# Optimization experiments

Measured on AMD Instinct MI355X. Metric: run time of the kernel, lower is better.

Reference implementation:

```python
import jax, jax.numpy as jnp
import numpy as np

B, S, D = 4, 2048, 1024
N_HEAD = 16
D_HEAD = D // N_HEAD
WINDOW = 1024
D_FF = 4 * D
EPS = 1e-5
NEG = -1e10


def _layernorm(x, g, b):
    mu = jnp.mean(x, axis=-1, keepdims=True)
    var = jnp.mean(jnp.square(x - mu), axis=-1, keepdims=True)
    return (x - mu) * jax.lax.rsqrt(var + EPS) * g + b


def setup_inputs() -> dict:
    key = jax.random.key(0)
    ks = jax.random.split(key, 12)
    s = 1.0 / np.sqrt(D)
    x = jax.random.normal(ks[0], (B, S, D), dtype=jnp.float32)
    key_pad_mask = jax.random.bernoulli(ks[1], 0.1, (B, S))
    return {
        "x": x,
        "key_pad_mask": key_pad_mask,
        "ln1_g": jnp.ones((D,), jnp.float32),
        "ln1_b": jnp.zeros((D,), jnp.float32),
        "wq": jax.random.normal(ks[2], (D, D), jnp.float32) * s,
        "bq": jnp.zeros((D,), jnp.float32),
        "wkv": jax.random.normal(ks[3], (D, 2 * D), jnp.float32) * s,
        "bkv": jnp.zeros((2 * D,), jnp.float32),
        "ln2_g": jnp.ones((D,), jnp.float32),
        "ln2_b": jnp.zeros((D,), jnp.float32),
        "w1": jax.random.normal(ks[4], (D, D_FF), jnp.float32) * s,
        "b1": jnp.zeros((D_FF,), jnp.float32),
        "w2": jax.random.normal(ks[5], (D_FF, D), jnp.float32) * (1.0 / np.sqrt(D_FF)),
        "b2": jnp.zeros((D,), jnp.float32),
    }


def reference(x, key_pad_mask, ln1_g, ln1_b, wq, bq, wkv, bkv, ln2_g, ln2_b, w1, b1, w2, b2):
    ln1x = _layernorm(x, ln1_g, ln1_b)
    # queries over full sequence: [B, S, nh, dh]
    q = (ln1x @ wq + bq).reshape(B, S, N_HEAD, D_HEAD)
    # keys/values from the last WINDOW tokens: [B, W, 2*nh, dh]
    kv = (ln1x[:, -WINDOW:, :] @ wkv + bkv).reshape(B, WINDOW, 2 * N_HEAD, D_HEAD)
    k, v = kv[..., :N_HEAD, :], kv[..., N_HEAD:, :]
    # NOTE: original scales by sqrt(embed_dim), not sqrt(head_dim)
    scores = jnp.einsum('bqhd,bkhd->bhqk', q, k) / np.sqrt(D)
    causal = jnp.triu(jnp.ones((S, WINDOW), dtype=bool), k=1)  # faithful to original
    pad = key_pad_mask[:, None, None, -WINDOW:]
    scores = jnp.where(pad | causal[None, None], jnp.float32(NEG), scores)
    attn = jax.nn.softmax(scores, axis=-1)
    out = jnp.einsum('bhqk,bkhd->bqhd', attn, v).reshape(B, S, D)
    h = _layernorm(out, ln2_g, ln2_b)
    h = jax.nn.silu(h @ w1 + b1) @ w2 + b2
    return h + x
```

## Files before the change

### kernel.cpp

```cpp
#include <hip/hip_runtime.h>
#include <hip/hip_bf16.h>

#define BB 4
#define SS 2048
#define DD 1024
#define HH 16
#define DHH 64
#define WW 1024
#define DFF 4096
#define MM (BB*SS)
#define NEGV (-1e10f)

using f32x4 = __attribute__((ext_vector_type(4))) float;
using s16x8 = __attribute__((ext_vector_type(8))) short;
using s16x4 = __attribute__((ext_vector_type(4))) short;

typedef const __attribute__((address_space(1))) void* gas_t;
typedef __attribute__((address_space(3))) void* las_t;

__device__ inline short f2b(float f) {
  __hip_bfloat16 h = __float2bfloat16(f);
  return __builtin_bit_cast(short, h);
}
__device__ inline float b2f(short u) {
  __hip_bfloat16 h = __builtin_bit_cast(__hip_bfloat16, u);
  return __bfloat162float(h);
}

__device__ inline void gload_lds16(const short* g, short* lds) {
  __builtin_amdgcn_global_load_lds((gas_t)g, (las_t)lds, 16, 0, 0);
}

__device__ inline f32x4 mfma16(s16x8 a, s16x8 b, f32x4 c) {
  return __builtin_amdgcn_mfma_f32_16x16x32_bf16(a, b, c, 0, 0, 0);
}

template<int IN_BF16>
__global__ __launch_bounds__(256) void ln_kernel(const void* __restrict__ inp,
                                                 const float* __restrict__ g,
                                                 const float* __restrict__ bta,
                                                 short* __restrict__ outp) {
  int row = blockIdx.x;
  int t = threadIdx.x;
  float v[4];
  if constexpr (IN_BF16) {
    s16x4 r4 = *((const s16x4*)((const short*)inp + (size_t)row*DD) + t);
    v[0]=b2f(r4[0]); v[1]=b2f(r4[1]); v[2]=b2f(r4[2]); v[3]=b2f(r4[3]);
  } else {
    f32x4 r4 = *((const f32x4*)((const float*)inp + (size_t)row*DD) + t);
    v[0]=r4[0]; v[1]=r4[1]; v[2]=r4[2]; v[3]=r4[3];
  }
  float s = v[0]+v[1]+v[2]+v[3];
  float sq = v[0]*v[0]+v[1]*v[1]+v[2]*v[2]+v[3]*v[3];
  for (int m=1;m<64;m<<=1){ s += __shfl_xor(s,m); sq += __shfl_xor(sq,m); }
  __shared__ float red[8];
  int wv = t>>6;
  if ((t&63)==0){ red[wv]=s; red[4+wv]=sq; }
  __syncthreads();
  s  = red[0]+red[1]+red[2]+red[3];
  sq = red[4]+red[5]+red[6]+red[7];
  float mean = s*(1.f/DD);
  float rstd = rsqrtf(sq*(1.f/DD) - mean*mean + 1e-5f);
  int col = t*4;
  s16x4 o;
  #pragma unroll
  for (int j=0;j<4;++j) o[j] = f2b((v[j]-mean)*rstd*g[col+j]+bta[col+j]);
  *((s16x4*)(outp + (size_t)row*DD) + t) = o;
}

__global__ __launch_bounds__(256) void transpose_cast(const float* __restrict__ in,
                                                      short* __restrict__ out,
                                                      int K, int N) {
  __shared__ float tile[32][33];
  int n0 = blockIdx.x*32, k0 = blockIdx.y*32;
  int tx = threadIdx.x & 31, ty = threadIdx.x >> 5;
  #pragma unroll
  for (int j=0;j<4;++j) tile[ty+8*j][tx] = in[(size_t)(k0+ty+8*j)*N + n0+tx];
  __syncthreads();
  #pragma unroll
  for (int j=0;j<4;++j) out[(size_t)(n0+ty+8*j)*K + k0+tx] = f2b(tile[tx][ty+8*j]);
}

template<int EPI>
__global__ __launch_bounds__(256) void gemm_bt(const short* __restrict__ A,
                                               const short* __restrict__ Bt,
                                               const float* __restrict__ bias,
                                               void* __restrict__ out1,
                                               void* __restrict__ out2,
                                               const float* __restrict__ resid,
                                               int N, int K) {
  __shared__ short As[128*32], Bs[128*32];
  int tid = threadIdx.x, l = tid&63;
  int wv = tid>>6, wm = wv>>1, wn = wv&1;
  int bx = blockIdx.x, by = blockIdx.y;
  const short* Ablk;
  if constexpr (EPI==1) {
    int b_ = (by*128)>>10;
    int w0 = (by*128)&1023;
    Ablk = A + ((size_t)b_*SS + (SS-WW) + w0)*DD;
  } else {
    Ablk = A + (size_t)by*128*K;
  }
  const short* Bblk = Bt + (size_t)bx*128*K;
  f32x4 acc[4][4];
  #pragma unroll
  for (int i=0;i<4;++i)
    #pragma unroll
    for(int j=0;j<4;++j)
      #pragma unroll
      for(int r=0;r<4;++r) acc[i][j][r]=0.f;
  int rA = l & 15;
  int cslot = (((l>>4) ^ ((l>>1)&3))*8);
  for (int kt=0; kt<K; kt+=32) {
    __syncthreads();
    #pragma unroll
    for (int p=0;p<2;++p) {
      int s = p*256 + tid;
      int srow = s>>2;
      int scs = (((s&3) ^ ((s>>3)&3))*8);
      gload_lds16(Ablk + (size_t)srow*K + kt + scs, &As[(p*256 + (tid & ~63))*8]);
      gload_lds16(Bblk + (size_t)srow*K + kt + scs, &Bs[(p*256 + (tid & ~63))*8]);
    }
    __syncthreads();
    s16x8 af[4], bfr[4];
    #pragma unroll
    for (int mf=0;mf<4;++mf) af[mf]  = *(const s16x8*)&As[(wm*64+mf*16+rA)*32 + cslot];
    #pragma unroll
    for (int nf=0;nf<4;++nf) bfr[nf] = *(const s16x8*)&Bs[(wn*64+nf*16+rA)*32 + cslot];
    #pragma unroll
    for (int mf=0;mf<4;++mf)
      #pragma unroll
      for (int nf=0;nf<4;++nf)
        acc[mf][nf] = mfma16(af[mf], bfr[nf], acc[mf][nf]);
  }
  #pragma unroll
  for (int mf=0;mf<4;++mf) {
    #pragma unroll
    for (int nf=0;nf<4;++nf) {
      #pragma unroll
      for (int r=0;r<4;++r) {
        int row = by*128 + wm*64 + mf*16 + ((l>>4)<<2) + r;
        int col = bx*128 + wn*64 + nf*16 + (l&15);
        float v = acc[mf][nf][r] + bias[col];
        if constexpr (EPI==0) {
          ((short*)out1)[(size_t)row*N + col] = f2b(v);
        } else if constexpr (EPI==1) {
          int b_ = row>>10, w_ = row&1023;
          if (col < DD) {
            int h = col>>6, dh = col&63;
            ((short*)out1)[(((size_t)(b_*HH+h))*WW + w_)*DHH + dh] = f2b(v);
          } else {
            int cc = col - DD;
            int h = cc>>6, dh = cc&63;
            ((short*)out2)[(((size_t)(b_*HH+h))*DHH + dh)*WW + w_] = f2b(v);
          }
        } else if constexpr (EPI==2) {
          float sv = v / (1.f + __expf(-v));
          ((short*)out1)[(size_t)row*N + col] = f2b(sv);
        } else {
          ((float*)out1)[(size_t)row*N + col] = v + resid[(size_t)row*N + col];
        }
      }
    }
  }
}

__global__ __launch_bounds__(256) void attn_kernel(const short* __restrict__ q,
    const short* __restrict__ kpan, const short* __restrict__ vtpan,
    const int* __restrict__ pad, short* __restrict__ outp) {
  __shared__ short Ks[64*64], Vts[64*64];
  __shared__ short P[4][16*72];
  int tid = threadIdx.x, l = tid&63, wv = tid>>6;
  int qt = blockIdx.x, h = blockIdx.y, bb = blockIdx.z;
  int s0 = qt*64;
  int srow0 = s0 + wv*16;
  const short* qbase = q + ((size_t)bb*SS + srow0 + (l&15))*DD + h*DHH + ((l>>4)*8);
  s16x8 aq0 = *(const s16x8*)qbase;
  s16x8 aq1 = *(const s16x8*)(qbase + 32);
  const short* kbase = kpan + (size_t)(bb*HH+h)*WW*DHH;
  const short* vbase = vtpan + (size_t)(bb*HH+h)*DHH*WW;
  const int* padb = pad + bb*SS + (SS-WW);
  f32x4 oacc[4];
  #pragma unroll
  for (int i=0;i<4;++i)
    #pragma unroll
    for (int r=0;r<4;++r) oacc[i][r]=0.f;
  float mrun[4], lrun[4];
  #pragma unroll
  for (int r=0;r<4;++r){ mrun[r]=-INFINITY; lrun[r]=0.f; }
  int nch = (qt+1 < 16) ? qt+1 : 16;

  auto body = [&](int c) {
    __syncthreads();
    #pragma unroll
    for (int p=0;p<2;++p) {
      int s = p*256 + tid;
      int row = s>>3;
      int scs = (((s&7) ^ (row&7))*8);
      gload_lds16(kbase + (size_t)(c*64+row)*DHH + scs, &Ks[(p*256 + (tid&~63))*8]);
      gload_lds16(vbase + (size_t)row*WW + c*64 + scs,  &Vts[(p*256 + (tid&~63))*8]);
    }
    __syncthreads();
    f32x4 sc[4];
    #pragma unroll
    for (int nf=0;nf<4;++nf)
      #pragma unroll
      for (int r=0;r<4;++r) sc[nf][r]=0.f;
    #pragma unroll
    for (int nf=0;nf<4;++nf) {
      int row = nf*16 + (l&15);
      s16x8 bk0 = *(const s16x8*)&Ks[row*64 + ((((l>>4)    ) ^ (l&7))*8)];
      s16x8 bk1 = *(const s16x8*)&Ks[row*64 + (((4 + (l>>4)) ^ (l&7))*8)];
      sc[nf] = mfma16(aq0, bk0, sc[nf]);
      sc[nf] = mfma16(aq1, bk1, sc[nf]);
    }
    float vals[4][4];
    float pm[4] = {-INFINITY,-INFINITY,-INFINITY,-INFINITY};
    #pragma unroll
    for (int nf=0;nf<4;++nf) {
      int j = c*64 + nf*16 + (l&15);
      int pd = padb[j];
      #pragma unroll
      for (int r=0;r<4;++r) {
        int sq_ = srow0 + ((l>>4)<<2) + r;
        float xv = (pd || (j > sq_)) ? NEGV : sc[nf][r]*0.03125f;
        vals[nf][r] = xv;
        pm[r] = fmaxf(pm[r], xv);
      }
    }
    #pragma unroll
    for (int m=1;m<16;m<<=1)
      #pragma unroll
      for (int r=0;r<4;++r) pm[r] = fmaxf(pm[r], __shfl_xor(pm[r], m));
    float scale[4], ls[4];
    #pragma unroll
    for (int r=0;r<4;++r) {
      float mn = fmaxf(mrun[r], pm[r]);
      scale[r] = __expf(mrun[r]-mn);
      mrun[r] = mn;
      ls[r] = 0.f;
    }
    #pragma unroll
    for (int nf=0;nf<4;++nf)
      #pragma unroll
      for (int r=0;r<4;++r) {
        float p_ = __expf(vals[nf][r]-mrun[r]);
        vals[nf][r]=p_; ls[r]+=p_;
      }
    #pragma unroll
    for (int m=1;m<16;m<<=1)
      #pragma unroll
      for (int r=0;r<4;++r) ls[r] += __shfl_xor(ls[r], m);
    #pragma unroll
    for (int r=0;r<4;++r) lrun[r] = lrun[r]*scale[r] + ls[r];
    #pragma unroll
    for (int nf=0;nf<4;++nf)
      #pragma unroll
      for (int r=0;r<4;++r) oacc[nf][r] *= scale[r];
    short* Pw = &P[wv][0];
    #pragma unroll
    for (int nf=0;nf<4;++nf)
      #pragma unroll
      for (int r=0;r<4;++r)
        Pw[(((l>>4)<<2)+r)*72 + nf*16 + (l&15)] = f2b(vals[nf][r]);
    #pragma unroll
    for (int ks=0;ks<2;++ks) {
      s16x8 ap = *(const s16x8*)&Pw[(l&15)*72 + ks*32 + ((l>>4)*8)];
      #pragma unroll
      for (int nf=0;nf<4;++nf) {
        int row = nf*16 + (l&15);
        s16x8 bv = *(const s16x8*)&Vts[row*64 + (((ks*4 + (l>>4)) ^ (l&7))*8)];
        oacc[nf] = mfma16(ap, bv, oacc[nf]);
      }
    }
  };

  for (int c=0;c<nch;++c) body(c);
  int dead = 0;
  #pragma unroll
  for (int r=0;r<4;++r) dead |= (mrun[r] < -5e9f) ? 1 : 0;
  if (__syncthreads_or(dead)) {
    for (int c=nch;c<16;++c) body(c);
  }
  #pragma unroll
  for (int nf=0;nf<4;++nf)
    #pragma unroll
    for (int r=0;r<4;++r) {
      int srow = srow0 + ((l>>4)<<2) + r;
      float o = oacc[nf][r] / lrun[r];
      outp[((size_t)bb*SS + srow)*DD + h*DHH + nf*16 + (l&15)] = f2b(o);
    }
}

extern "C" void kernel_launch(void* const* d_in, const int* in_sizes, int n_in,
                              void* d_out, int out_size, void* d_ws, size_t ws_size,
                              hipStream_t stream) {
  const float* x    = (const float*)d_in[0];
  const int*   pad  = (const int*)d_in[1];
  const float* ln1g = (const float*)d_in[2];
  const float* ln1b = (const float*)d_in[3];
  const float* wq   = (const float*)d_in[4];
  const float* bq   = (const float*)d_in[5];
  const float* wkv  = (const float*)d_in[6];
  const float* bkv  = (const float*)d_in[7];
  const float* ln2g = (const float*)d_in[8];
  const float* ln2b = (const float*)d_in[9];
  const float* w1   = (const float*)d_in[10];
  const float* b1   = (const float*)d_in[11];
  const float* w2   = (const float*)d_in[12];
  const float* b2   = (const float*)d_in[13];

  char* ws = (char*)d_ws;
  const size_t MB = 1024*1024;
  short* ln1x = (short*)(ws + 0);
  short* qb   = (short*)(ws + 16*MB);
  short* kpan = (short*)(ws + 32*MB);
  short* vtp  = (short*)(ws + 40*MB);
  short* h1   = (short*)(ws + 0);
  short* outb = (short*)(ws + 64*MB);
  short* hb   = (short*)(ws + 80*MB);
  short* wqT  = (short*)(ws + 96*MB);
  short* wkvT = (short*)(ws + 98*MB);
  short* w1T  = (short*)(ws + 102*MB);
  short* w2T  = (short*)(ws + 110*MB);

  transpose_cast<<<dim3(32,32),  256,0,stream>>>(wq,  wqT,  1024, 1024);
  transpose_cast<<<dim3(64,32),  256,0,stream>>>(wkv, wkvT, 1024, 2048);
  transpose_cast<<<dim3(128,32), 256,0,stream>>>(w1,  w1T,  1024, 4096);
  transpose_cast<<<dim3(32,128), 256,0,stream>>>(w2,  w2T,  4096, 1024);
  ln_kernel<0><<<MM,256,0,stream>>>(x, ln1g, ln1b, ln1x);
  gemm_bt<0><<<dim3(8,64), 256,0,stream>>>(ln1x, wqT,  bq,  qb,   nullptr, nullptr, 1024, 1024);
  gemm_bt<1><<<dim3(16,32),256,0,stream>>>(ln1x, wkvT, bkv, kpan, vtp,     nullptr, 2048, 1024);
  attn_kernel<<<dim3(32,16,4),256,0,stream>>>(qb, kpan, vtp, pad, outb);
  ln_kernel<1><<<MM,256,0,stream>>>(outb, ln2g, ln2b, hb);
  gemm_bt<2><<<dim3(32,64),256,0,stream>>>(hb, w1T, b1, h1,    nullptr, nullptr, 4096, 1024);
  gemm_bt<3><<<dim3(8,64), 256,0,stream>>>(h1, w2T, b2, d_out, nullptr, x,       1024, 4096);
}
```

Baseline: 451.2 us.

## Restructure attention: 128-row query tiles, double-buffered K/V, pad bitmask, heavy-first order

The attention kernel now gives each block 128 query rows (32 per wave, in two 16-row groups), so every K/V chunk loaded into LDS feeds twice as many MFMAs. K/V chunks are double-buffered, with the next chunk's async global-to-LDS load issued before computing on the current one. The padding mask is packed into per-lane 64-bit bitmasks by a small pre-kernel, which replaces per-element global int loads. Causal masking is applied only on diagonal chunks, blocks run in reverse order so the heaviest tiles launch first, and s_setprio hints wrap the MFMA sections. The cost is higher register and LDS use and half as many blocks, which may lower occupancy.

```diff
diff --git a/kernel.cpp b/kernel.cpp
--- a/kernel.cpp
+++ b/kernel.cpp
@@ -14,6 +14,7 @@
 using f32x4 = __attribute__((ext_vector_type(4))) float;
 using s16x8 = __attribute__((ext_vector_type(8))) short;
 using s16x4 = __attribute__((ext_vector_type(4))) short;
+using u64 = unsigned long long;
 
 typedef const __attribute__((address_space(1))) void* gas_t;
 typedef __attribute__((address_space(3))) void* las_t;
@@ -79,6 +80,17 @@
   __syncthreads();
   #pragma unroll
   for (int j=0;j<4;++j) out[(size_t)(n0+ty+8*j)*K + k0+tx] = f2b(tile[tx][ty+8*j]);
+}
+
+__global__ void pad_bitmask(const int* __restrict__ pad, u64* __restrict__ pm) {
+  int idx = threadIdx.x;
+  int b_ = idx>>4, col = idx&15;
+  const int* pb = pad + b_*SS + (SS-WW);
+  u64 m = 0;
+  for (int c=0;c<16;++c)
+    for (int nf=0;nf<4;++nf)
+      if (pb[c*64+nf*16+col]) m |= (1ull << (c*4+nf));
+  pm[idx] = m;
 }
 
 template<int EPI>
@@ -167,129 +179,189 @@
 
 __global__ __launch_bounds__(256) void attn_kernel(const short* __restrict__ q,
     const short* __restrict__ kpan, const short* __restrict__ vtpan,
-    const int* __restrict__ pad, short* __restrict__ outp) {
-  __shared__ short Ks[64*64], Vts[64*64];
-  __shared__ short P[4][16*72];
+    const u64* __restrict__ pmarr, short* __restrict__ outp) {
+  __shared__ short Ks[2][64*64], Vts[2][64*64];
+  __shared__ short P[4][32*72];
   int tid = threadIdx.x, l = tid&63, wv = tid>>6;
-  int qt = blockIdx.x, h = blockIdx.y, bb = blockIdx.z;
-  int s0 = qt*64;
-  int srow0 = s0 + wv*16;
-  const short* qbase = q + ((size_t)bb*SS + srow0 + (l&15))*DD + h*DHH + ((l>>4)*8);
-  s16x8 aq0 = *(const s16x8*)qbase;
-  s16x8 aq1 = *(const s16x8*)(qbase + 32);
+  int t = 15 - blockIdx.x;
+  int h = blockIdx.y, bb = blockIdx.z;
+  int s0 = t*128;
+  int r0 = s0 + wv*32;
   const short* kbase = kpan + (size_t)(bb*HH+h)*WW*DHH;
   const short* vbase = vtpan + (size_t)(bb*HH+h)*DHH*WW;
-  const int* padb = pad + bb*SS + (SS-WW);
-  f32x4 oacc[4];
-  #pragma unroll
-  for (int i=0;i<4;++i)
-    #pragma unroll
-    for (int r=0;r<4;++r) oacc[i][r]=0.f;
-  float mrun[4], lrun[4];
-  #pragma unroll
-  for (int r=0;r<4;++r){ mrun[r]=-INFINITY; lrun[r]=0.f; }
-  int nch = (qt+1 < 16) ? qt+1 : 16;
-
-  auto body = [&](int c) {
-    __syncthreads();
+  u64 pmask = pmarr[bb*16 + (l&15)];
+  s16x8 aq[2][2];
+  #pragma unroll
+  for (int g=0;g<2;++g)
+    #pragma unroll
+    for (int kf=0;kf<2;++kf)
+      aq[g][kf] = *(const s16x8*)(q + ((size_t)bb*SS + r0 + g*16 + (l&15))*DD
+                                    + h*DHH + (l>>4)*8 + kf*32);
+  f32x4 oacc[2][4];
+  float mrun[2][4], lrun[2][4];
+  #pragma unroll
+  for (int g=0;g<2;++g)
+    #pragma unroll
+    for (int i=0;i<4;++i) {
+      #pragma unroll
+      for (int r=0;r<4;++r) oacc[g][i][r]=0.f;
+      mrun[g][i]=-INFINITY; lrun[g][i]=0.f;
+    }
+  int nch = 2*t+2 < 16 ? 2*t+2 : 16;
+
+  auto stage = [&](int c, int bi) {
     #pragma unroll
     for (int p=0;p<2;++p) {
       int s = p*256 + tid;
       int row = s>>3;
       int scs = (((s&7) ^ (row&7))*8);
-      gload_lds16(kbase + (size_t)(c*64+row)*DHH + scs, &Ks[(p*256 + (tid&~63))*8]);
-      gload_lds16(vbase + (size_t)row*WW + c*64 + scs,  &Vts[(p*256 + (tid&~63))*8]);
-    }
-    __syncthreads();
-    f32x4 sc[4];
-    #pragma unroll
-    for (int nf=0;nf<4;++nf)
-      #pragma unroll
-      for (int r=0;r<4;++r) sc[nf][r]=0.f;
+      gload_lds16(kbase + (size_t)(c*64+row)*DHH + scs, &Ks[bi][(p*256 + (tid&~63))*8]);
+      gload_lds16(vbase + (size_t)row*WW + c*64 + scs,  &Vts[bi][(p*256 + (tid&~63))*8]);
+    }
+  };
+
+  auto compute = [&](int c, int bi) {
+    f32x4 sc[2][4];
+    #pragma unroll
+    for (int g=0;g<2;++g)
+      #pragma unroll
+      for (int nf=0;nf<4;++nf)
+        #pragma unroll
+        for (int r=0;r<4;++r) sc[g][nf][r]=0.f;
+    __builtin_amdgcn_s_setprio(1);
     #pragma unroll
     for (int nf=0;nf<4;++nf) {
       int row = nf*16 + (l&15);
-      s16x8 bk0 = *(const s16x8*)&Ks[row*64 + ((((l>>4)    ) ^ (l&7))*8)];
-      s16x8 bk1 = *(const s16x8*)&Ks[row*64 + (((4 + (l>>4)) ^ (l&7))*8)];
-      sc[nf] = mfma16(aq0, bk0, sc[nf]);
-      sc[nf] = mfma16(aq1, bk1, sc[nf]);
-    }
-    float vals[4][4];
-    float pm[4] = {-INFINITY,-INFINITY,-INFINITY,-INFINITY};
+      s16x8 bk0 = *(const s16x8*)&Ks[bi][row*64 + ((((l>>4)    ) ^ (l&7))*8)];
+      s16x8 bk1 = *(const s16x8*)&Ks[bi][row*64 + (((4 + (l>>4)) ^ (l&7))*8)];
+      #pragma unroll
+      for (int g=0;g<2;++g) {
+        sc[g][nf] = mfma16(aq[g][0], bk0, sc[g][nf]);
+        sc[g][nf] = mfma16(aq[g][1], bk1, sc[g][nf]);
+      }
+    }
+    __builtin_amdgcn_s_setprio(0);
+    int diag = (c >= 2*t);
+    float pm[2][4];
+    #pragma unroll
+    for (int g=0;g<2;++g)
+      #pragma unroll
+      for (int r=0;r<4;++r) pm[g][r] = -INFINITY;
     #pragma unroll
     for (int nf=0;nf<4;++nf) {
       int j = c*64 + nf*16 + (l&15);
-      int pd = padb[j];
+      int padj = (int)((pmask >> (c*4+nf)) & 1ull);
+      #pragma unroll
+      for (int g=0;g<2;++g)
+        #pragma unroll
+        for (int r=0;r<4;++r) {
+          float xv = padj ? NEGV : sc[g][nf][r]*0.03125f;
+          if (diag) {
+            int sq_ = r0 + g*16 + ((l>>4)<<2) + r;
+            xv = (j > sq_) ? NEGV : xv;
+          }
+          sc[g][nf][r] = xv;
+          pm[g][r] = fmaxf(pm[g][r], xv);
+        }
+    }
+    #pragma unroll
+    for (int m=1;m<16;m<<=1)
+      #pragma unroll
+      for (int g=0;g<2;++g)
+        #pragma unroll
+        for (int r=0;r<4;++r) pm[g][r] = fmaxf(pm[g][r], __shfl_xor(pm[g][r], m));
+    float scale[2][4], ls[2][4];
+    #pragma unroll
+    for (int g=0;g<2;++g)
       #pragma unroll
       for (int r=0;r<4;++r) {
-        int sq_ = srow0 + ((l>>4)<<2) + r;
-        float xv = (pd || (j > sq_)) ? NEGV : sc[nf][r]*0.03125f;
-        vals[nf][r] = xv;
-        pm[r] = fmaxf(pm[r], xv);
+        float mn = fmaxf(mrun[g][r], pm[g][r]);
+        scale[g][r] = __expf(mrun[g][r]-mn);
+        mrun[g][r] = mn;
+        ls[g][r] = 0.f;
       }
-    }
+    #pragma unroll
+    for (int nf=0;nf<4;++nf)
+      #pragma unroll
+      for (int g=0;g<2;++g)
+        #pragma unroll
+        for (int r=0;r<4;++r) {
+          float p_ = __expf(sc[g][nf][r]-mrun[g][r]);
+          sc[g][nf][r]=p_; ls[g][r]+=p_;
+        }
     #pragma unroll
     for (int m=1;m<16;m<<=1)
       #pragma unroll
-      for (int r=0;r<4;++r) pm[r] = fmaxf(pm[r], __shfl_xor(pm[r], m));
-    float scale[4], ls[4];
-    #pragma unroll
-    for (int r=0;r<4;++r) {
-      float mn = fmaxf(mrun[r], pm[r]);
-      scale[r] = __expf(mrun[r]-mn);
-      mrun[r] = mn;
-      ls[r] = 0.f;
-    }
-    #pragma unroll
-    for (int nf=0;nf<4;++nf)
-      #pragma unroll
-      for (int r=0;r<4;++r) {
-        float p_ = __expf(vals[nf][r]-mrun[r]);
-        vals[nf][r]=p_; ls[r]+=p_;
-      }
-    #pragma unroll
-    for (int m=1;m<16;m<<=1)
-      #pragma unroll
-      for (int r=0;r<4;++r) ls[r] += __shfl_xor(ls[r], m);
-    #pragma unroll
-    for (int r=0;r<4;++r) lrun[r] = lrun[r]*scale[r] + ls[r];
-    #pragma unroll
-    for (int nf=0;nf<4;++nf)
-      #pragma unroll
-      for (int r=0;r<4;++r) oacc[nf][r] *= scale[r];
+      for (int g=0;g<2;++g)
+        #pragma unroll
+        for (int r=0;r<4;++r) ls[g][r] += __shfl_xor(ls[g][r], m);
+    #pragma unroll
+    for (int g=0;g<2;++g)
+      #pragma unroll
+      for (int r=0;r<4;++r) lrun[g][r] = lrun[g][r]*scale[g][r] + ls[g][r];
+    #pragma unroll
+    for (int g=0;g<2;++g)
+      #pragma unroll
+      for (int nf=0;nf<4;++nf)
+        #pragma unroll
+        for (int r=0;r<4;++r) oacc[g][nf][r] *= scale[g][r];
     short* Pw = &P[wv][0];
     #pragma unroll
-    for (int nf=0;nf<4;++nf)
-      #pragma unroll
-      for (int r=0;r<4;++r)
-        Pw[(((l>>4)<<2)+r)*72 + nf*16 + (l&15)] = f2b(vals[nf][r]);
+    for (int g=0;g<2;++g)
+      #pragma unroll
+      for (int nf=0;nf<4;++nf)
+        #pragma unroll
+        for (int r=0;r<4;++r)
+          Pw[(g*16+((l>>4)<<2)+r)*72 + nf*16 + (l&15)] = f2b(sc[g][nf][r]);
+    __builtin_amdgcn_s_setprio(1);
     #pragma unroll
     for (int ks=0;ks<2;++ks) {
-      s16x8 ap = *(const s16x8*)&Pw[(l&15)*72 + ks*32 + ((l>>4)*8)];
+      s16x8 ap[2];
+      #pragma unroll
+      for (int g=0;g<2;++g)
+        ap[g] = *(const s16x8*)&Pw[(g*16+(l&15))*72 + ks*32 + ((l>>4)*8)];
       #pragma unroll
       for (int nf=0;nf<4;++nf) {
         int row = nf*16 + (l&15);
-        s16x8 bv = *(const s16x8*)&Vts[row*64 + (((ks*4 + (l>>4)) ^ (l&7))*8)];
-        oacc[nf] = mfma16(ap, bv, oacc[nf]);
+        s16x8 bv = *(const s16x8*)&Vts[bi][row*64 + (((ks*4 + (l>>4)) ^ (l&7))*8)];
+        #pragma unroll
+        for (int g=0;g<2;++g)
+          oacc[g][nf] = mfma16(ap[g], bv, oacc[g][nf]);
       }
     }
+    __builtin_amdgcn_s_setprio(0);
   };
 
-  for (int c=0;c<nch;++c) body(c);
+  stage(0, 0);
+  __syncthreads();
+  for (int c=0;c<nch;++c) {
+    if (c+1 < nch) stage(c+1, (c+1)&1);
+    compute(c, c&1);
+    __syncthreads();
+  }
   int dead = 0;
   #pragma unroll
-  for (int r=0;r<4;++r) dead |= (mrun[r] < -5e9f) ? 1 : 0;
+  for (int g=0;g<2;++g)
+    #pragma unroll
+    for (int r=0;r<4;++r) dead |= (mrun[g][r] < -5e9f) ? 1 : 0;
   if (__syncthreads_or(dead)) {
-    for (int c=nch;c<16;++c) body(c);
-  }
-  #pragma unroll
-  for (int nf=0;nf<4;++nf)
-    #pragma unroll
-    for (int r=0;r<4;++r) {
-      int srow = srow0 + ((l>>4)<<2) + r;
-      float o = oacc[nf][r] / lrun[r];
-      outp[((size_t)bb*SS + srow)*DD + h*DHH + nf*16 + (l&15)] = f2b(o);
-    }
+    for (int c=nch;c<16;++c) {
+      stage(c, c&1);
+      __syncthreads();
+      compute(c, c&1);
+      __syncthreads();
+    }
+  }
+  #pragma unroll
+  for (int g=0;g<2;++g)
+    #pragma unroll
+    for (int nf=0;nf<4;++nf)
+      #pragma unroll
+      for (int r=0;r<4;++r) {
+        int srow = r0 + g*16 + ((l>>4)<<2) + r;
+        float o = oacc[g][nf][r] / lrun[g][r];
+        outp[((size_t)bb*SS + srow)*DD + h*DHH + nf*16 + (l&15)] = f2b(o);
+      }
 }
 
 extern "C" void kernel_launch(void* const* d_in, const int* in_sizes, int n_in,
@@ -316,6 +388,7 @@
   short* qb   = (short*)(ws + 16*MB);
   short* kpan = (short*)(ws + 32*MB);
   short* vtp  = (short*)(ws + 40*MB);
+  u64*   pmar = (u64*)  (ws + 48*MB);
   short* h1   = (short*)(ws + 0);
   short* outb = (short*)(ws + 64*MB);
   short* hb   = (short*)(ws + 80*MB);
@@ -324,6 +397,7 @@
   short* w1T  = (short*)(ws + 102*MB);
   short* w2T  = (short*)(ws + 110*MB);
 
+  pad_bitmask<<<1,64,0,stream>>>(pad, pmar);
   transpose_cast<<<dim3(32,32),  256,0,stream>>>(wq,  wqT,  1024, 1024);
   transpose_cast<<<dim3(64,32),  256,0,stream>>>(wkv, wkvT, 1024, 2048);
   transpose_cast<<<dim3(128,32), 256,0,stream>>>(w1,  w1T,  1024, 4096);
@@ -331,7 +405,7 @@
   ln_kernel<0><<<MM,256,0,stream>>>(x, ln1g, ln1b, ln1x);
   gemm_bt<0><<<dim3(8,64), 256,0,stream>>>(ln1x, wqT,  bq,  qb,   nullptr, nullptr, 1024, 1024);
   gemm_bt<1><<<dim3(16,32),256,0,stream>>>(ln1x, wkvT, bkv, kpan, vtp,     nullptr, 2048, 1024);
-  attn_kernel<<<dim3(32,16,4),256,0,stream>>>(qb, kpan, vtp, pad, outb);
+  attn_kernel<<<dim3(16,16,4),256,0,stream>>>(qb, kpan, vtp, pmar, outb);
   ln_kernel<1><<<MM,256,0,stream>>>(outb, ln2g, ln2b, hb);
   gemm_bt<2><<<dim3(32,64),256,0,stream>>>(hb, w1T, b1, h1,    nullptr, nullptr, 4096, 1024);
   gemm_bt<3><<<dim3(8,64), 256,0,stream>>>(h1, w2T, b2, d_out, nullptr, x,       1024, 4096);
```

Result: slower. 461.2 us (+2.2%).
